# Performance work log

Measured on AMD Instinct MI355X. Metric: run time of the kernel, lower is better.

The kernel has to match this reference:

```python
import jax, jax.numpy as jnp
import numpy as np

N_EMBD = 1024
HEAD_SIZE = 64  # n_embd // n_head = 1024 // 16


def setup_inputs() -> dict:
    key = jax.random.key(0)
    ks = jax.random.split(key, 7)
    B, T, C, H = 4, 2048, N_EMBD, HEAD_SIZE
    s = 1.0 / np.sqrt(C)
    return {
        "x": jax.random.normal(ks[0], (B, T, C), dtype=jnp.float32),
        "Wq": jax.random.normal(ks[1], (C, H), dtype=jnp.float32) * s,
        "bq": jax.random.normal(ks[2], (H,), dtype=jnp.float32) * 0.01,
        "Wk": jax.random.normal(ks[3], (C, H), dtype=jnp.float32) * s,
        "bk": jax.random.normal(ks[4], (H,), dtype=jnp.float32) * 0.01,
        "Wv": jax.random.normal(ks[5], (C, H), dtype=jnp.float32) * s,
        "bv": jax.random.normal(ks[6], (H,), dtype=jnp.float32) * 0.01,
    }


def reference(x, Wq, bq, Wk, bk, Wv, bv):
    # x: [B, T, C]
    B, T, C = x.shape
    q = x @ Wq + bq  # [B, T, H]
    k = x @ Wk + bk  # [B, T, H]
    v = x @ Wv + bv  # [B, T, H]
    # NOTE: original module does NOT scale by 1/sqrt(head_size)
    wei = jnp.einsum("bth,bsh->bts", q, k)  # [B, T, T]
    causal = jnp.tril(jnp.ones((T, T), dtype=bool))
    wei = jnp.where(causal, wei, -jnp.inf)
    wei = jax.nn.softmax(wei, axis=-1)
    out = jnp.einsum("bts,bsh->bth", wei, v)  # [B, T, H]
    return out
```

## Files before the change

kernel.cpp:

```cpp
#include <hip/hip_runtime.h>

typedef float f32x4 __attribute__((ext_vector_type(4)));
typedef short s16x4 __attribute__((ext_vector_type(4)));
typedef short s16x8 __attribute__((ext_vector_type(8)));

#define LOG2E 1.4426950408889634f

__device__ __forceinline__ short f2bf(float f) {
  unsigned u = __float_as_uint(f);
  unsigned r = (u + 0x7fffu + ((u >> 16) & 1u)) >> 16;
  return (short)r;
}
__device__ __forceinline__ float bf2f(short s) {
  return __uint_as_float(((unsigned)(unsigned short)s) << 16);
}
__device__ __forceinline__ unsigned cvt_pk_bf16(float a, float b) {
  unsigned r;
  asm("v_cvt_pk_bf16_f32 %0, %1, %2" : "=v"(r) : "v"(a), "v"(b));
  return r;
}

__device__ __forceinline__ f32x4 mfma16(s16x4 a, s16x4 b, f32x4 c) {
  return __builtin_amdgcn_mfma_f32_16x16x16bf16_1k(a, b, c, 0, 0, 0);
}
__device__ __forceinline__ f32x4 mfma32(s16x8 a, s16x8 b, f32x4 c) {
  return __builtin_amdgcn_mfma_f32_16x16x32_bf16(a, b, c, 0, 0, 0);
}

__device__ __forceinline__ void gl_lds16(const void* gp, void* sp) {
  __builtin_amdgcn_global_load_lds(
      (__attribute__((address_space(1))) void*)const_cast<void*>(gp),
      (__attribute__((address_space(3))) void*)sp, 16, 0, 0);
}

__global__ __launch_bounds__(256) void prep_w(
    const float* __restrict__ Wq, const float* __restrict__ Wk, const float* __restrict__ Wv,
    short* __restrict__ wt_hi, short* __restrict__ wt_lo) {
  int idx = blockIdx.x * 256 + threadIdx.x;
  int n = idx >> 10;
  int c = idx & 1023;
  const float* W = (n < 64) ? Wq : ((n < 128) ? Wk : Wv);
  float v = W[c * 64 + (n & 63)];
  short hi = f2bf(v);
  short lo = f2bf(v - bf2f(hi));
  wt_hi[idx] = hi;
  wt_lo[idx] = lo;
}

__global__ __launch_bounds__(512, 2) void proj_qkv(
    const float* __restrict__ x,
    const short* __restrict__ wt_hi, const short* __restrict__ wt_lo,
    const float* __restrict__ bq, const float* __restrict__ bk, const float* __restrict__ bv,
    short* __restrict__ q_hi, short* __restrict__ q_lo,
    short* __restrict__ k_hi, short* __restrict__ k_lo,
    short* __restrict__ v_t) {
  const int tid = threadIdx.x;
  const int lane = tid & 63;
  const int wv = tid >> 6;
  const int col = lane & 15;
  const int g = lane >> 4;
  const int mg = wv >> 2;
  const int ng = wv & 3;
  const int tokbase = blockIdx.x * 32;

  __shared__ short lds[5][12288];

  const int wsl = ((lane & 3) ^ ((lane >> 3) & 3)) * 8;
  const short* s0 = wt_hi + (size_t)(16 * wv + (lane >> 2)) * 1024 + wsl;
  const int d0 = wv * 512;
  const int c1 = wv + 8;
  const short* s1 = (c1 < 12 ? wt_hi + (size_t)(16 * c1 + (lane >> 2)) * 1024
                             : wt_lo + (size_t)(16 * (c1 - 12) + (lane >> 2)) * 1024) + wsl;
  const int d1 = (c1 < 12) ? c1 * 512 : 6144 + (c1 - 12) * 512;
  const int c2 = wv + 16;
  const bool isx = (c2 >= 20);
  const short* s2 = isx
      ? (const short*)(x + (size_t)(tokbase + 8 * (c2 - 20) + (lane >> 3)) * 1024 +
                       ((lane & 7) ^ (lane >> 3)) * 4)
      : wt_lo + (size_t)(16 * (c2 - 12) + (lane >> 2)) * 1024 + wsl;
  const int d2 = isx ? 10240 + (c2 - 20) * 512 : 6144 + (c2 - 12) * 512;
  const int st2 = isx ? 64 : 32;

#define STAGE(BP, S) do { \
    gl_lds16(s0 + (S) * 32, (BP) + d0); \
    gl_lds16(s1 + (S) * 32, (BP) + d1); \
    gl_lds16(s2 + (S) * st2, (BP) + d2); \
  } while (0)

#define PIPE_WAIT(N) do { \
    asm volatile("s_waitcnt vmcnt(" #N ")" ::: "memory"); \
    __builtin_amdgcn_s_barrier(); \
    __builtin_amdgcn_sched_barrier(0); \
  } while (0)
#define PIPE_END do { \
    asm volatile("s_waitcnt lgkmcnt(0)" ::: "memory"); \
    __builtin_amdgcn_sched_barrier(0); \
    __builtin_amdgcn_s_barrier(); \
  } while (0)

  const int arow = mg * 16 + col;
  const int xq0 = ((2 * g) ^ (arow & 7)) << 2;
  const int xq1 = ((2 * g + 1) ^ (arow & 7)) << 2;
  const int rq = ng * 16 + col;
  const int ws = (g ^ ((rq >> 1) & 3)) << 3;

  f32x4 accQ = {0,0,0,0}, accK = {0,0,0,0}, accV = {0,0,0,0};

  typedef union { unsigned u[4]; s16x8 v8; } pk8;

#define COMPUTE(BP) do { \
    const short* bp_ = (BP); \
    const float* xb_ = (const float*)(bp_ + 10240); \
    f32x4 x0_ = *(const f32x4*)(xb_ + arow * 32 + xq0); \
    f32x4 x1_ = *(const f32x4*)(xb_ + arow * 32 + xq1); \
    pk8 xh_, xl_; \
    xh_.u[0] = cvt_pk_bf16(x0_[0], x0_[1]); \
    xh_.u[1] = cvt_pk_bf16(x0_[2], x0_[3]); \
    xh_.u[2] = cvt_pk_bf16(x1_[0], x1_[1]); \
    xh_.u[3] = cvt_pk_bf16(x1_[2], x1_[3]); \
    xl_.u[0] = cvt_pk_bf16(x0_[0] - __uint_as_float(xh_.u[0] << 16), \
                           x0_[1] - __uint_as_float(xh_.u[0] & 0xffff0000u)); \
    xl_.u[1] = cvt_pk_bf16(x0_[2] - __uint_as_float(xh_.u[1] << 16), \
                           x0_[3] - __uint_as_float(xh_.u[1] & 0xffff0000u)); \
    xl_.u[2] = cvt_pk_bf16(x1_[0] - __uint_as_float(xh_.u[2] << 16), \
                           x1_[1] - __uint_as_float(xh_.u[2] & 0xffff0000u)); \
    xl_.u[3] = cvt_pk_bf16(x1_[2] - __uint_as_float(xh_.u[3] << 16), \
                           x1_[3] - __uint_as_float(xh_.u[3] & 0xffff0000u)); \
    s16x8 qh_ = *(const s16x8*)(bp_ + rq * 32 + ws); \
    s16x8 kh_ = *(const s16x8*)(bp_ + (64 + rq) * 32 + ws); \
    s16x8 vh_ = *(const s16x8*)(bp_ + (128 + rq) * 32 + ws); \
    s16x8 ql_ = *(const s16x8*)(bp_ + 6144 + rq * 32 + ws); \
    s16x8 kl_ = *(const s16x8*)(bp_ + 6144 + (64 + rq) * 32 + ws); \
    accQ = mfma32(xh_.v8, qh_, accQ); \
    accK = mfma32(xh_.v8, kh_, accK); \
    accV = mfma32(xh_.v8, vh_, accV); \
    accQ = mfma32(xl_.v8, qh_, accQ); \
    accK = mfma32(xl_.v8, kh_, accK); \
    accQ = mfma32(xh_.v8, ql_, accQ); \
    accK = mfma32(xh_.v8, kl_, accK); \
  } while (0)

  short* cA = &lds[0][0];
  short* cB = &lds[1][0];
  short* cC = &lds[2][0];
  short* cD = &lds[3][0];
  short* cE = &lds[4][0];

  STAGE(cA, 0); STAGE(cB, 1); STAGE(cC, 2); STAGE(cD, 3);

#pragma unroll 1
  for (int b = 0; b < 28; ++b) {
    STAGE(cE, b + 4);
    PIPE_WAIT(12);
    COMPUTE(cA);
    PIPE_END;
    short* t = cA; cA = cB; cB = cC; cC = cD; cD = cE; cE = t;
  }
  PIPE_WAIT(9); COMPUTE(cA); PIPE_END;
  PIPE_WAIT(6); COMPUTE(cB); PIPE_END;
  PIPE_WAIT(3); COMPUTE(cC); PIPE_END;
  PIPE_WAIT(0); COMPUTE(cD);

  {
    const int hQ = ng * 16 + col;
    const float biasq = bq[hQ];
    const float biask = bk[hQ];
    const float biasv = bv[hQ];
#pragma unroll
    for (int r = 0; r < 4; ++r) {
      const int tok = tokbase + mg * 16 + 4 * g + r;
      float fq = accQ[r] + biasq;
      short qh = f2bf(fq);
      q_hi[(size_t)tok * 64 + hQ] = qh;
      q_lo[(size_t)tok * 64 + hQ] = f2bf(fq - bf2f(qh));
      float fk = accK[r] + biask;
      short kh = f2bf(fk);
      k_hi[(size_t)tok * 64 + hQ] = kh;
      k_lo[(size_t)tok * 64 + hQ] = f2bf(fk - bf2f(kh));
      const int bb = tok >> 11;
      const int tl = tok & 2047;
      v_t[((size_t)bb * 64 + hQ) * 2048 + tl] = f2bf(accV[r] + biasv);
    }
  }
#undef STAGE
#undef PIPE_WAIT
#undef PIPE_END
#undef COMPUTE
}

__global__ __launch_bounds__(256) void attn(
    const short* __restrict__ q_hi, const short* __restrict__ q_lo,
    const short* __restrict__ k_hi, const short* __restrict__ k_lo,
    const short* __restrict__ v_t,
    float* __restrict__ pm, float* __restrict__ pl, float* __restrict__ pO) {
  const int tid = threadIdx.x;
  const int lane = tid & 63;
  const int w = tid >> 6;
  const int col = lane & 15;
  const int g = lane >> 4;
  const int bid = blockIdx.x;
  const int p = bid & 31;
  const int b = (bid >> 5) & 3;
  const int s = bid >> 7;
  const int kb0 = 512 * s;
  if (kb0 > 64 * p + 63) return;
  const int S = (((64 * p + 63 - kb0) >> 5) + 1) < 16
                    ? (((64 * p + 63 - kb0) >> 5) + 1) : 16;

  __shared__ short lds[2][6144];

  const int qlo = 64 * p + 16 * w;

  const short* qbh = q_hi + (size_t)(b * 2048 + qlo + col) * 64 + g * 8;
  const short* qbl = q_lo + (size_t)(b * 2048 + qlo + col) * 64 + g * 8;
  s16x8 qh0 = *(const s16x8*)(qbh);
  s16x8 qh1 = *(const s16x8*)(qbh + 32);
  s16x8 ql0 = *(const s16x8*)(qbl);
  s16x8 ql1 = *(const s16x8*)(qbl + 32);
  asm volatile("" : "+v"(qh0), "+v"(qh1), "+v"(ql0), "+v"(ql1));

  f32x4 o0 = {0,0,0,0}, o1 = {0,0,0,0}, o2 = {0,0,0,0}, o3 = {0,0,0,0};
  float m = -3.0e38f, l = 0.0f;

  const int kr32 = 8 * w + (lane >> 3);
  const int ksl = ((lane & 7) ^ (lane >> 3)) * 8;
  const short* khs = k_hi + (size_t)(b * 2048 + kb0 + kr32) * 64 + ksl;
  const short* kls = k_lo + (size_t)(b * 2048 + kb0 + kr32) * 64 + ksl;
  const int vh_r = 16 * w + (lane >> 2);
  const int vsl = ((2 * (lane & 3)) ^ (vh_r & 6)) * 4;
  const short* vs = v_t + ((size_t)b * 64 + vh_r) * 2048 + kb0 + vsl;

#define STAGE(J) do { \
    short* bp_ = &lds[(J) & 1][0]; \
    gl_lds16(khs + (J) * 32 * 64, bp_ + w * 512); \
    gl_lds16(kls + (J) * 32 * 64, bp_ + 2048 + w * 512); \
    gl_lds16(vs + (J) * 32, bp_ + 4096 + w * 512); \
  } while (0)

  const int cx = col & 7;
  const int kslot0 = (g ^ cx) << 3;
  const int kslot1 = ((4 + g) ^ cx) << 3;
  const int vg0 = ((g) ^ (col & 6)) << 2;
  const int vg1 = ((4 + g) ^ (col & 6)) << 2;

#define SUBTILE(BP, KG0, VGOFF) do { \
    const short* kr_ = (BP) + ((KG0)&31) * 64 + col * 64; \
    s16x8 kh0_ = *(const s16x8*)(kr_ + kslot0); \
    s16x8 kh1_ = *(const s16x8*)(kr_ + kslot1); \
    s16x8 kl0_ = *(const s16x8*)(kr_ + 2048 + kslot0); \
    s16x8 kl1_ = *(const s16x8*)(kr_ + 2048 + kslot1); \
    f32x4 u1_ = {0,0,0,0}, u2_ = {0,0,0,0}; \
    u1_ = mfma32(kh0_, qh0, u1_); u1_ = mfma32(kh1_, qh1, u1_); \
    u2_ = mfma32(kh0_, ql0, u2_); u2_ = mfma32(kh1_, ql1, u2_); \
    u2_ = mfma32(kl0_, qh0, u2_); u2_ = mfma32(kl1_, qh1, u2_); \
    f32x4 s_ = u1_ + u2_; \
    if ((KG0) == qlo) { \
      _Pragma("unroll") for (int i = 0; i < 4; ++i) \
        if (4 * g + i > col) s_[i] = -3.0e38f; \
    } \
    float mx_ = fmaxf(fmaxf(s_[0], s_[1]), fmaxf(s_[2], s_[3])); \
    mx_ = fmaxf(mx_, __shfl_xor(mx_, 16)); \
    mx_ = fmaxf(mx_, __shfl_xor(mx_, 32)); \
    const float mn_ = fmaxf(m, mx_); \
    const float rs_ = __builtin_amdgcn_exp2f((m - mn_) * LOG2E); \
    const float p0_ = __builtin_amdgcn_exp2f((s_[0] - mn_) * LOG2E); \
    const float p1_ = __builtin_amdgcn_exp2f((s_[1] - mn_) * LOG2E); \
    const float p2_ = __builtin_amdgcn_exp2f((s_[2] - mn_) * LOG2E); \
    const float p3_ = __builtin_amdgcn_exp2f((s_[3] - mn_) * LOG2E); \
    l = l * rs_ + (p0_ + p1_ + p2_ + p3_); \
    o0 *= rs_; o1 *= rs_; o2 *= rs_; o3 *= rs_; \
    m = mn_; \
    s16x4 pb_; \
    pb_[0] = f2bf(p0_); pb_[1] = f2bf(p1_); pb_[2] = f2bf(p2_); pb_[3] = f2bf(p3_); \
    const short* vb_ = (BP) + 4096 + col * 32 + (VGOFF); \
    o0 = mfma16(*(const s16x4*)(vb_),        pb_, o0); \
    o1 = mfma16(*(const s16x4*)(vb_ + 512),  pb_, o1); \
    o2 = mfma16(*(const s16x4*)(vb_ + 1024), pb_, o2); \
    o3 = mfma16(*(const s16x4*)(vb_ + 1536), pb_, o3); \
  } while (0)

#define COMPUTE(J) do { \
    const int kb_ = kb0 + 32 * (J); \
    if (kb_ <= qlo + 15) { \
      const short* bp_ = &lds[(J) & 1][0]; \
      SUBTILE(bp_, kb_, vg0); \
      if (kb_ + 16 <= qlo + 15) SUBTILE(bp_, kb_ + 16, vg1); \
    } \
  } while (0)

  STAGE(0);
  __syncthreads();
#pragma unroll 1
  for (int j = 0; j < S; ++j) {
    if (j + 1 < S) STAGE(j + 1);
    COMPUTE(j);
    __syncthreads();
  }

  l += __shfl_xor(l, 16);
  l += __shfl_xor(l, 32);
  const int row = b * 2048 + qlo + col;
  if (g == 0) {
    pm[s * 8192 + row] = m;
    pl[s * 8192 + row] = l;
  }
  {
    float* d = pO + ((size_t)s * 8192 + row) * 64 + 4 * g;
    *(f32x4*)(d)      = o0;
    *(f32x4*)(d + 16) = o1;
    *(f32x4*)(d + 32) = o2;
    *(f32x4*)(d + 48) = o3;
  }
#undef STAGE
#undef SUBTILE
#undef COMPUTE
}

__global__ __launch_bounds__(256) void reduce_p(
    const float* __restrict__ pm, const float* __restrict__ pl,
    const float* __restrict__ pO, float* __restrict__ out) {
  const int idx = blockIdx.x * 256 + threadIdx.x;
  const int row = idx >> 4;
  const int hq = (idx & 15) * 4;
  const int smax = (row & 2047) >> 9;
  float M = -3.0e38f;
  for (int s = 0; s <= smax; ++s) M = fmaxf(M, pm[s * 8192 + row]);
  float L = 0.f;
  f32x4 acc = {0, 0, 0, 0};
  for (int s = 0; s <= smax; ++s) {
    const float ws = __builtin_amdgcn_exp2f((pm[s * 8192 + row] - M) * LOG2E);
    L += ws * pl[s * 8192 + row];
    f32x4 ov = *(const f32x4*)(pO + ((size_t)s * 8192 + row) * 64 + hq);
    acc += ov * ws;
  }
  const float invL = 1.0f / L;
  *(f32x4*)(out + (size_t)row * 64 + hq) = acc * invL;
}

extern "C" void kernel_launch(void* const* d_in, const int* in_sizes, int n_in,
                              void* d_out, int out_size, void* d_ws, size_t ws_size,
                              hipStream_t stream) {
  const float* x  = (const float*)d_in[0];
  const float* Wq = (const float*)d_in[1];
  const float* bq = (const float*)d_in[2];
  const float* Wk = (const float*)d_in[3];
  const float* bk = (const float*)d_in[4];
  const float* Wv = (const float*)d_in[5];
  const float* bv = (const float*)d_in[6];
  float* out = (float*)d_out;

  char* ws = (char*)d_ws;
  short* wt_hi = (short*)(ws);
  short* wt_lo = (short*)(ws + 393216);
  short* q_hi  = (short*)(ws + 786432);
  short* q_lo  = (short*)(ws + 786432 + 1048576);
  short* k_hi  = (short*)(ws + 786432 + 2 * 1048576);
  short* k_lo  = (short*)(ws + 786432 + 3 * 1048576);
  short* v_t   = (short*)(ws + 786432 + 4 * 1048576);
  float* pm    = (float*)(ws + 6029312);
  float* pl    = (float*)(ws + 6160384);
  float* pO    = (float*)(ws + 6291456);

  hipLaunchKernelGGL(prep_w, dim3(768), dim3(256), 0, stream, Wq, Wk, Wv, wt_hi, wt_lo);
  hipLaunchKernelGGL(proj_qkv, dim3(256), dim3(512), 0, stream,
                     x, wt_hi, wt_lo, bq, bk, bv, q_hi, q_lo, k_hi, k_lo, v_t);
  hipLaunchKernelGGL(attn, dim3(512), dim3(256), 0, stream,
                     q_hi, q_lo, k_hi, k_lo, v_t, pm, pl, pO);
  hipLaunchKernelGGL(reduce_p, dim3(512), dim3(256), 0, stream, pm, pl, pO, out);
}
```

Measured before the change: 57.57 us.

## Split attention into two-pass softmax kernel writing P and separate PV kernel

Replaces the flash-style online-softmax attention plus split-K reduction with two kernels. The first computes QK scores twice, once to find the per-warp row max and again to write bf16 exponentials to a materialized P buffer in global memory along with per-warp max and sum. The second multiplies P by V and merges the 8 warp partials through LDS. This removes the rescaling of O on every tile and the separate reduce kernel, but it doubles the QK MFMA work, drops LDS staging of K/V, and adds a large P write and read through global memory.

Measured after the change: 86.99 us. 51.1% more time.

```diff
diff --git a/kernel.cpp b/kernel.cpp
--- a/kernel.cpp
+++ b/kernel.cpp
@@ -188,153 +188,202 @@
 #undef COMPUTE
 }
 
-__global__ __launch_bounds__(256) void attn(
+__global__ __launch_bounds__(512) void qk_p(
     const short* __restrict__ q_hi, const short* __restrict__ q_lo,
     const short* __restrict__ k_hi, const short* __restrict__ k_lo,
-    const short* __restrict__ v_t,
-    float* __restrict__ pm, float* __restrict__ pl, float* __restrict__ pO) {
+    short* __restrict__ P, float* __restrict__ pm, float* __restrict__ pl) {
   const int tid = threadIdx.x;
   const int lane = tid & 63;
   const int w = tid >> 6;
   const int col = lane & 15;
   const int g = lane >> 4;
-  const int bid = blockIdx.x;
-  const int p = bid & 31;
-  const int b = (bid >> 5) & 3;
-  const int s = bid >> 7;
-  const int kb0 = 512 * s;
-  if (kb0 > 64 * p + 63) return;
-  const int S = (((64 * p + 63 - kb0) >> 5) + 1) < 16
-                    ? (((64 * p + 63 - kb0) >> 5) + 1) : 16;
-
-  __shared__ short lds[2][6144];
-
-  const int qlo = 64 * p + 16 * w;
-
-  const short* qbh = q_hi + (size_t)(b * 2048 + qlo + col) * 64 + g * 8;
-  const short* qbl = q_lo + (size_t)(b * 2048 + qlo + col) * 64 + g * 8;
-  s16x8 qh0 = *(const s16x8*)(qbh);
-  s16x8 qh1 = *(const s16x8*)(qbh + 32);
-  s16x8 ql0 = *(const s16x8*)(qbl);
-  s16x8 ql1 = *(const s16x8*)(qbl + 32);
-  asm volatile("" : "+v"(qh0), "+v"(qh1), "+v"(ql0), "+v"(ql1));
-
-  f32x4 o0 = {0,0,0,0}, o1 = {0,0,0,0}, o2 = {0,0,0,0}, o3 = {0,0,0,0};
-  float m = -3.0e38f, l = 0.0f;
-
-  const int kr32 = 8 * w + (lane >> 3);
-  const int ksl = ((lane & 7) ^ (lane >> 3)) * 8;
-  const short* khs = k_hi + (size_t)(b * 2048 + kb0 + kr32) * 64 + ksl;
-  const short* kls = k_lo + (size_t)(b * 2048 + kb0 + kr32) * 64 + ksl;
-  const int vh_r = 16 * w + (lane >> 2);
-  const int vsl = ((2 * (lane & 3)) ^ (vh_r & 6)) * 4;
-  const short* vs = v_t + ((size_t)b * 64 + vh_r) * 2048 + kb0 + vsl;
-
-#define STAGE(J) do { \
-    short* bp_ = &lds[(J) & 1][0]; \
-    gl_lds16(khs + (J) * 32 * 64, bp_ + w * 512); \
-    gl_lds16(kls + (J) * 32 * 64, bp_ + 2048 + w * 512); \
-    gl_lds16(vs + (J) * 32, bp_ + 4096 + w * 512); \
-  } while (0)
-
-  const int cx = col & 7;
-  const int kslot0 = (g ^ cx) << 3;
-  const int kslot1 = ((4 + g) ^ cx) << 3;
-  const int vg0 = ((g) ^ (col & 6)) << 2;
-  const int vg1 = ((4 + g) ^ (col & 6)) << 2;
-
-#define SUBTILE(BP, KG0, VGOFF) do { \
-    const short* kr_ = (BP) + ((KG0)&31) * 64 + col * 64; \
-    s16x8 kh0_ = *(const s16x8*)(kr_ + kslot0); \
-    s16x8 kh1_ = *(const s16x8*)(kr_ + kslot1); \
-    s16x8 kl0_ = *(const s16x8*)(kr_ + 2048 + kslot0); \
-    s16x8 kl1_ = *(const s16x8*)(kr_ + 2048 + kslot1); \
+  const int T = 63 - (blockIdx.x >> 2);
+  const int b = blockIdx.x & 3;
+  const int t0 = 2 * T, t1 = 2 * T + 1;
+
+  const short* q0h = q_hi + (size_t)(b * 2048 + t0 * 16 + col) * 64 + g * 8;
+  const short* q0l = q_lo + (size_t)(b * 2048 + t0 * 16 + col) * 64 + g * 8;
+  s16x8 qh00 = *(const s16x8*)(q0h);
+  s16x8 qh01 = *(const s16x8*)(q0h + 32);
+  s16x8 ql00 = *(const s16x8*)(q0l);
+  s16x8 ql01 = *(const s16x8*)(q0l + 32);
+  s16x8 qh10 = *(const s16x8*)(q0h + 16 * 64);
+  s16x8 qh11 = *(const s16x8*)(q0h + 16 * 64 + 32);
+  s16x8 ql10 = *(const s16x8*)(q0l + 16 * 64);
+  s16x8 ql11 = *(const s16x8*)(q0l + 16 * 64 + 32);
+  asm volatile("" : "+v"(qh00), "+v"(qh01), "+v"(ql00), "+v"(ql01));
+  asm volatile("" : "+v"(qh10), "+v"(qh11), "+v"(ql10), "+v"(ql11));
+
+#define SCORES(OUT, QH0, QH1, QL0, QL1, TT, KT) do { \
     f32x4 u1_ = {0,0,0,0}, u2_ = {0,0,0,0}; \
-    u1_ = mfma32(kh0_, qh0, u1_); u1_ = mfma32(kh1_, qh1, u1_); \
-    u2_ = mfma32(kh0_, ql0, u2_); u2_ = mfma32(kh1_, ql1, u2_); \
-    u2_ = mfma32(kl0_, qh0, u2_); u2_ = mfma32(kl1_, qh1, u2_); \
-    f32x4 s_ = u1_ + u2_; \
-    if ((KG0) == qlo) { \
+    u1_ = mfma32(kh0_, QH0, u1_); u1_ = mfma32(kh1_, QH1, u1_); \
+    u2_ = mfma32(kh0_, QL0, u2_); u2_ = mfma32(kh1_, QL1, u2_); \
+    u2_ = mfma32(kl0_, QH0, u2_); u2_ = mfma32(kl1_, QH1, u2_); \
+    OUT = u1_ + u2_; \
+    if ((KT) == (TT)) { \
       _Pragma("unroll") for (int i = 0; i < 4; ++i) \
-        if (4 * g + i > col) s_[i] = -3.0e38f; \
+        if (4 * g + i > col) OUT[i] = -3.0e38f; \
     } \
-    float mx_ = fmaxf(fmaxf(s_[0], s_[1]), fmaxf(s_[2], s_[3])); \
-    mx_ = fmaxf(mx_, __shfl_xor(mx_, 16)); \
-    mx_ = fmaxf(mx_, __shfl_xor(mx_, 32)); \
-    const float mn_ = fmaxf(m, mx_); \
-    const float rs_ = __builtin_amdgcn_exp2f((m - mn_) * LOG2E); \
-    const float p0_ = __builtin_amdgcn_exp2f((s_[0] - mn_) * LOG2E); \
-    const float p1_ = __builtin_amdgcn_exp2f((s_[1] - mn_) * LOG2E); \
-    const float p2_ = __builtin_amdgcn_exp2f((s_[2] - mn_) * LOG2E); \
-    const float p3_ = __builtin_amdgcn_exp2f((s_[3] - mn_) * LOG2E); \
-    l = l * rs_ + (p0_ + p1_ + p2_ + p3_); \
-    o0 *= rs_; o1 *= rs_; o2 *= rs_; o3 *= rs_; \
-    m = mn_; \
-    s16x4 pb_; \
-    pb_[0] = f2bf(p0_); pb_[1] = f2bf(p1_); pb_[2] = f2bf(p2_); pb_[3] = f2bf(p3_); \
-    const short* vb_ = (BP) + 4096 + col * 32 + (VGOFF); \
-    o0 = mfma16(*(const s16x4*)(vb_),        pb_, o0); \
-    o1 = mfma16(*(const s16x4*)(vb_ + 512),  pb_, o1); \
-    o2 = mfma16(*(const s16x4*)(vb_ + 1024), pb_, o2); \
-    o3 = mfma16(*(const s16x4*)(vb_ + 1536), pb_, o3); \
-  } while (0)
-
-#define COMPUTE(J) do { \
-    const int kb_ = kb0 + 32 * (J); \
-    if (kb_ <= qlo + 15) { \
-      const short* bp_ = &lds[(J) & 1][0]; \
-      SUBTILE(bp_, kb_, vg0); \
-      if (kb_ + 16 <= qlo + 15) SUBTILE(bp_, kb_ + 16, vg1); \
+  } while (0)
+
+  float m0 = -3.0e38f, m1 = -3.0e38f;
+
+#pragma unroll 1
+  for (int kt = w; kt <= t1; kt += 8) {
+    const short* krh = k_hi + (size_t)(b * 2048 + kt * 16 + col) * 64 + g * 8;
+    const short* krl = k_lo + (size_t)(b * 2048 + kt * 16 + col) * 64 + g * 8;
+    s16x8 kh0_ = *(const s16x8*)(krh);
+    s16x8 kh1_ = *(const s16x8*)(krh + 32);
+    s16x8 kl0_ = *(const s16x8*)(krl);
+    s16x8 kl1_ = *(const s16x8*)(krl + 32);
+    f32x4 s_;
+    SCORES(s_, qh10, qh11, ql10, ql11, t1, kt);
+    m1 = fmaxf(m1, fmaxf(fmaxf(s_[0], s_[1]), fmaxf(s_[2], s_[3])));
+    if (kt <= t0) {
+      SCORES(s_, qh00, qh01, ql00, ql01, t0, kt);
+      m0 = fmaxf(m0, fmaxf(fmaxf(s_[0], s_[1]), fmaxf(s_[2], s_[3])));
+    }
+  }
+  m0 = fmaxf(m0, __shfl_xor(m0, 16));
+  m0 = fmaxf(m0, __shfl_xor(m0, 32));
+  m1 = fmaxf(m1, __shfl_xor(m1, 16));
+  m1 = fmaxf(m1, __shfl_xor(m1, 32));
+
+  float lw0 = 0.0f, lw1 = 0.0f;
+
+#pragma unroll 1
+  for (int kt = w; kt <= t1; kt += 8) {
+    const short* krh = k_hi + (size_t)(b * 2048 + kt * 16 + col) * 64 + g * 8;
+    const short* krl = k_lo + (size_t)(b * 2048 + kt * 16 + col) * 64 + g * 8;
+    s16x8 kh0_ = *(const s16x8*)(krh);
+    s16x8 kh1_ = *(const s16x8*)(krh + 32);
+    s16x8 kl0_ = *(const s16x8*)(krl);
+    s16x8 kl1_ = *(const s16x8*)(krl + 32);
+    f32x4 s_;
+    __builtin_amdgcn_s_setprio(1);
+    SCORES(s_, qh10, qh11, ql10, ql11, t1, kt);
+    __builtin_amdgcn_s_setprio(0);
+    {
+      const float p0 = __builtin_amdgcn_exp2f((s_[0] - m1) * LOG2E);
+      const float p1 = __builtin_amdgcn_exp2f((s_[1] - m1) * LOG2E);
+      const float p2 = __builtin_amdgcn_exp2f((s_[2] - m1) * LOG2E);
+      const float p3 = __builtin_amdgcn_exp2f((s_[3] - m1) * LOG2E);
+      lw1 += p0 + p1 + p2 + p3;
+      s16x4 pb;
+      pb[0] = f2bf(p0); pb[1] = f2bf(p1); pb[2] = f2bf(p2); pb[3] = f2bf(p3);
+      *(s16x4*)(P + ((size_t)((b * 128 + t1) * 128 + kt)) * 256 + col * 16 + 4 * g) = pb;
+    }
+    if (kt <= t0) {
+      __builtin_amdgcn_s_setprio(1);
+      SCORES(s_, qh00, qh01, ql00, ql01, t0, kt);
+      __builtin_amdgcn_s_setprio(0);
+      const float p0 = __builtin_amdgcn_exp2f((s_[0] - m0) * LOG2E);
+      const float p1 = __builtin_amdgcn_exp2f((s_[1] - m0) * LOG2E);
+      const float p2 = __builtin_amdgcn_exp2f((s_[2] - m0) * LOG2E);
+      const float p3 = __builtin_amdgcn_exp2f((s_[3] - m0) * LOG2E);
+      lw0 += p0 + p1 + p2 + p3;
+      s16x4 pb;
+      pb[0] = f2bf(p0); pb[1] = f2bf(p1); pb[2] = f2bf(p2); pb[3] = f2bf(p3);
+      *(s16x4*)(P + ((size_t)((b * 128 + t0) * 128 + kt)) * 256 + col * 16 + 4 * g) = pb;
+    }
+  }
+  lw0 += __shfl_xor(lw0, 16); lw0 += __shfl_xor(lw0, 32);
+  lw1 += __shfl_xor(lw1, 16); lw1 += __shfl_xor(lw1, 32);
+
+  if (g == 0) {
+    pm[w * 8192 + b * 2048 + t0 * 16 + col] = m0;
+    pl[w * 8192 + b * 2048 + t0 * 16 + col] = lw0;
+    pm[w * 8192 + b * 2048 + t1 * 16 + col] = m1;
+    pl[w * 8192 + b * 2048 + t1 * 16 + col] = lw1;
+  }
+#undef SCORES
+}
+
+__global__ __launch_bounds__(512) void pv(
+    const short* __restrict__ P, const short* __restrict__ v_t,
+    const float* __restrict__ pm, const float* __restrict__ pl,
+    float* __restrict__ out) {
+  const int tid = threadIdx.x;
+  const int lane = tid & 63;
+  const int w = tid >> 6;
+  const int col = lane & 15;
+  const int g = lane >> 4;
+  const int T = 63 - (blockIdx.x >> 2);
+  const int b = blockIdx.x & 3;
+  const int t0 = 2 * T, t1 = 2 * T + 1;
+
+  __shared__ float ldsO[8 * 64 * 17];
+
+  f32x4 o00 = {0,0,0,0}, o01 = {0,0,0,0}, o02 = {0,0,0,0}, o03 = {0,0,0,0};
+  f32x4 o10 = {0,0,0,0}, o11 = {0,0,0,0}, o12 = {0,0,0,0}, o13 = {0,0,0,0};
+
+  const short* vbase = v_t + ((size_t)b * 64 + col) * 2048 + 4 * g;
+
+#pragma unroll 1
+  for (int kt = w; kt <= t1; kt += 8) {
+    const short* vr = vbase + 16 * kt;
+    s16x4 v0 = *(const s16x4*)(vr);
+    s16x4 v1 = *(const s16x4*)(vr + 16 * 2048);
+    s16x4 v2 = *(const s16x4*)(vr + 32 * 2048);
+    s16x4 v3 = *(const s16x4*)(vr + 48 * 2048);
+    s16x4 pb1 = *(const s16x4*)(P + ((size_t)((b * 128 + t1) * 128 + kt)) * 256 + col * 16 + 4 * g);
+    __builtin_amdgcn_s_setprio(1);
+    o10 = mfma16(v0, pb1, o10);
+    o11 = mfma16(v1, pb1, o11);
+    o12 = mfma16(v2, pb1, o12);
+    o13 = mfma16(v3, pb1, o13);
+    __builtin_amdgcn_s_setprio(0);
+    if (kt <= t0) {
+      s16x4 pb0 = *(const s16x4*)(P + ((size_t)((b * 128 + t0) * 128 + kt)) * 256 + col * 16 + 4 * g);
+      __builtin_amdgcn_s_setprio(1);
+      o00 = mfma16(v0, pb0, o00);
+      o01 = mfma16(v1, pb0, o01);
+      o02 = mfma16(v2, pb0, o02);
+      o03 = mfma16(v3, pb0, o03);
+      __builtin_amdgcn_s_setprio(0);
+    }
+  }
+
+#define MERGE(TT, O0, O1, O2, O3) do { \
+    _Pragma("unroll") \
+    for (int r = 0; r < 4; ++r) { \
+      ldsO[(w * 64 +  0 + 4 * g + r) * 17 + col] = O0[r]; \
+      ldsO[(w * 64 + 16 + 4 * g + r) * 17 + col] = O1[r]; \
+      ldsO[(w * 64 + 32 + 4 * g + r) * 17 + col] = O2[r]; \
+      ldsO[(w * 64 + 48 + 4 * g + r) * 17 + col] = O3[r]; \
     } \
-  } while (0)
-
-  STAGE(0);
-  __syncthreads();
-#pragma unroll 1
-  for (int j = 0; j < S; ++j) {
-    if (j + 1 < S) STAGE(j + 1);
-    COMPUTE(j);
-    __syncthreads();
-  }
-
-  l += __shfl_xor(l, 16);
-  l += __shfl_xor(l, 32);
-  const int row = b * 2048 + qlo + col;
-  if (g == 0) {
-    pm[s * 8192 + row] = m;
-    pl[s * 8192 + row] = l;
-  }
-  {
-    float* d = pO + ((size_t)s * 8192 + row) * 64 + 4 * g;
-    *(f32x4*)(d)      = o0;
-    *(f32x4*)(d + 16) = o1;
-    *(f32x4*)(d + 32) = o2;
-    *(f32x4*)(d + 48) = o3;
-  }
-#undef STAGE
-#undef SUBTILE
-#undef COMPUTE
-}
-
-__global__ __launch_bounds__(256) void reduce_p(
-    const float* __restrict__ pm, const float* __restrict__ pl,
-    const float* __restrict__ pO, float* __restrict__ out) {
-  const int idx = blockIdx.x * 256 + threadIdx.x;
-  const int row = idx >> 4;
-  const int hq = (idx & 15) * 4;
-  const int smax = (row & 2047) >> 9;
-  float M = -3.0e38f;
-  for (int s = 0; s <= smax; ++s) M = fmaxf(M, pm[s * 8192 + row]);
-  float L = 0.f;
-  f32x4 acc = {0, 0, 0, 0};
-  for (int s = 0; s <= smax; ++s) {
-    const float ws = __builtin_amdgcn_exp2f((pm[s * 8192 + row] - M) * LOG2E);
-    L += ws * pl[s * 8192 + row];
-    f32x4 ov = *(const f32x4*)(pO + ((size_t)s * 8192 + row) * 64 + hq);
-    acc += ov * ws;
-  }
-  const float invL = 1.0f / L;
-  *(f32x4*)(out + (size_t)row * 64 + hq) = acc * invL;
+    __syncthreads(); \
+    { \
+      const int q = tid >> 5;           \
+      const int h0 = tid & 31;          \
+      const int row = b * 2048 + (TT) * 16 + q; \
+      float mw[8], lw[8]; \
+      _Pragma("unroll") \
+      for (int u = 0; u < 8; ++u) { mw[u] = pm[u * 8192 + row]; lw[u] = pl[u * 8192 + row]; } \
+      float M = mw[0]; \
+      _Pragma("unroll") for (int u = 1; u < 8; ++u) M = fmaxf(M, mw[u]); \
+      float ew[8]; float L = 0.0f; \
+      _Pragma("unroll") \
+      for (int u = 0; u < 8; ++u) { \
+        ew[u] = __builtin_amdgcn_exp2f((mw[u] - M) * LOG2E); \
+        L += ew[u] * lw[u]; \
+      } \
+      const float invL = 1.0f / L; \
+      _Pragma("unroll") \
+      for (int e = 0; e < 2; ++e) { \
+        const int h = h0 + 32 * e; \
+        float acc = 0.0f; \
+        _Pragma("unroll") \
+        for (int u = 0; u < 8; ++u) acc += ew[u] * ldsO[(u * 64 + h) * 17 + q]; \
+        out[(size_t)row * 64 + h] = acc * invL; \
+      } \
+    } \
+    __syncthreads(); \
+  } while (0)
+
+  MERGE(t0, o00, o01, o02, o03);
+  MERGE(t1, o10, o11, o12, o13);
+#undef MERGE
 }
 
 extern "C" void kernel_launch(void* const* d_in, const int* in_sizes, int n_in,
@@ -357,14 +406,15 @@
   short* k_hi  = (short*)(ws + 786432 + 2 * 1048576);
   short* k_lo  = (short*)(ws + 786432 + 3 * 1048576);
   short* v_t   = (short*)(ws + 786432 + 4 * 1048576);
-  float* pm    = (float*)(ws + 6029312);
-  float* pl    = (float*)(ws + 6160384);
-  float* pO    = (float*)(ws + 6291456);
+  short* Pbuf  = (short*)(ws + 6029312);
+  float* pm    = (float*)(ws + 39583744);
+  float* pl    = (float*)(ws + 39845888);
 
   hipLaunchKernelGGL(prep_w, dim3(768), dim3(256), 0, stream, Wq, Wk, Wv, wt_hi, wt_lo);
   hipLaunchKernelGGL(proj_qkv, dim3(256), dim3(512), 0, stream,
                      x, wt_hi, wt_lo, bq, bk, bv, q_hi, q_lo, k_hi, k_lo, v_t);
-  hipLaunchKernelGGL(attn, dim3(512), dim3(256), 0, stream,
-                     q_hi, q_lo, k_hi, k_lo, v_t, pm, pl, pO);
-  hipLaunchKernelGGL(reduce_p, dim3(512), dim3(256), 0, stream, pm, pl, pO, out);
-}
+  hipLaunchKernelGGL(qk_p, dim3(256), dim3(512), 0, stream,
+                     q_hi, q_lo, k_hi, k_lo, Pbuf, pm, pl);
+  hipLaunchKernelGGL(pv, dim3(256), dim3(512), 0, stream,
+                     Pbuf, v_t, pm, pl, out);
+}
```

## Split attention into per-wave 128-key chunks reading K/V directly from global memory

Applied to the files above, without the earlier changes.

Rewrites the attention kernel so each wave independently handles one 16-row query tile against one 128-key chunk (8 subtiles), with 16 chunks per row instead of 4. The LDS double-buffered staging and block barriers are removed, and K and V are loaded straight from global memory, relying on cache reuse across waves. Fully masked chunks write neutral partials, and the reduction and workspace offsets are resized for 16 splits. This exposes much more parallelism and removes sync, at the cost of more partial-output traffic in the reduce step and uncoalesced, uncached-in-LDS global loads.

Result: slower. 106.6 us (+85.2%).

```diff
diff --git a/kernel.cpp b/kernel.cpp
--- a/kernel.cpp
+++ b/kernel.cpp
@@ -193,26 +193,35 @@
     const short* __restrict__ k_hi, const short* __restrict__ k_lo,
     const short* __restrict__ v_t,
     float* __restrict__ pm, float* __restrict__ pl, float* __restrict__ pO) {
-  const int tid = threadIdx.x;
-  const int lane = tid & 63;
-  const int w = tid >> 6;
+  const int lane = threadIdx.x & 63;
+  const int w = threadIdx.x >> 6;
   const int col = lane & 15;
   const int g = lane >> 4;
-  const int bid = blockIdx.x;
-  const int p = bid & 31;
-  const int b = (bid >> 5) & 3;
-  const int s = bid >> 7;
-  const int kb0 = 512 * s;
-  if (kb0 > 64 * p + 63) return;
-  const int S = (((64 * p + 63 - kb0) >> 5) + 1) < 16
-                    ? (((64 * p + 63 - kb0) >> 5) + 1) : 16;
-
-  __shared__ short lds[2][6144];
-
-  const int qlo = 64 * p + 16 * w;
-
-  const short* qbh = q_hi + (size_t)(b * 2048 + qlo + col) * 64 + g * 8;
-  const short* qbl = q_lo + (size_t)(b * 2048 + qlo + col) * 64 + g * 8;
+  const int W = blockIdx.x * 4 + w;
+  const int c = W & 15;
+  const int t = (W >> 4) & 127;
+  const int b = W >> 11;
+  const int kbase = b * 2048;
+  const int row = kbase + t * 16 + col;
+  float* dO = pO + ((size_t)c * 8192 + row) * 64 + 4 * g;
+
+  if (8 * c > t) {
+    if (g == 0) {
+      pm[c * 8192 + row] = -3.0e38f;
+      pl[c * 8192 + row] = 0.0f;
+    }
+    const f32x4 z = {0.f, 0.f, 0.f, 0.f};
+    *(f32x4*)(dO)      = z;
+    *(f32x4*)(dO + 16) = z;
+    *(f32x4*)(dO + 32) = z;
+    *(f32x4*)(dO + 48) = z;
+    return;
+  }
+  const int ks0 = 8 * c;
+  const int ks1 = (8 * c + 7 < t) ? 8 * c + 7 : t;
+
+  const short* qbh = q_hi + (size_t)(row) * 64 + g * 8;
+  const short* qbl = q_lo + (size_t)(row) * 64 + g * 8;
   s16x8 qh0 = *(const s16x8*)(qbh);
   s16x8 qh1 = *(const s16x8*)(qbh + 32);
   s16x8 ql0 = *(const s16x8*)(qbl);
@@ -222,98 +231,65 @@
   f32x4 o0 = {0,0,0,0}, o1 = {0,0,0,0}, o2 = {0,0,0,0}, o3 = {0,0,0,0};
   float m = -3.0e38f, l = 0.0f;
 
-  const int kr32 = 8 * w + (lane >> 3);
-  const int ksl = ((lane & 7) ^ (lane >> 3)) * 8;
-  const short* khs = k_hi + (size_t)(b * 2048 + kb0 + kr32) * 64 + ksl;
-  const short* kls = k_lo + (size_t)(b * 2048 + kb0 + kr32) * 64 + ksl;
-  const int vh_r = 16 * w + (lane >> 2);
-  const int vsl = ((2 * (lane & 3)) ^ (vh_r & 6)) * 4;
-  const short* vs = v_t + ((size_t)b * 64 + vh_r) * 2048 + kb0 + vsl;
-
-#define STAGE(J) do { \
-    short* bp_ = &lds[(J) & 1][0]; \
-    gl_lds16(khs + (J) * 32 * 64, bp_ + w * 512); \
-    gl_lds16(kls + (J) * 32 * 64, bp_ + 2048 + w * 512); \
-    gl_lds16(vs + (J) * 32, bp_ + 4096 + w * 512); \
-  } while (0)
-
-  const int cx = col & 7;
-  const int kslot0 = (g ^ cx) << 3;
-  const int kslot1 = ((4 + g) ^ cx) << 3;
-  const int vg0 = ((g) ^ (col & 6)) << 2;
-  const int vg1 = ((4 + g) ^ (col & 6)) << 2;
-
-#define SUBTILE(BP, KG0, VGOFF) do { \
-    const short* kr_ = (BP) + ((KG0)&31) * 64 + col * 64; \
-    s16x8 kh0_ = *(const s16x8*)(kr_ + kslot0); \
-    s16x8 kh1_ = *(const s16x8*)(kr_ + kslot1); \
-    s16x8 kl0_ = *(const s16x8*)(kr_ + 2048 + kslot0); \
-    s16x8 kl1_ = *(const s16x8*)(kr_ + 2048 + kslot1); \
-    f32x4 u1_ = {0,0,0,0}, u2_ = {0,0,0,0}; \
-    u1_ = mfma32(kh0_, qh0, u1_); u1_ = mfma32(kh1_, qh1, u1_); \
-    u2_ = mfma32(kh0_, ql0, u2_); u2_ = mfma32(kh1_, ql1, u2_); \
-    u2_ = mfma32(kl0_, qh0, u2_); u2_ = mfma32(kl1_, qh1, u2_); \
-    f32x4 s_ = u1_ + u2_; \
-    if ((KG0) == qlo) { \
-      _Pragma("unroll") for (int i = 0; i < 4; ++i) \
-        if (4 * g + i > col) s_[i] = -3.0e38f; \
+#define SUBTILE(KT) do { \
+    if ((KT) <= ks1) { \
+      const short* krh_ = k_hi + (size_t)(kbase + (KT) * 16 + col) * 64 + g * 8; \
+      const short* krl_ = k_lo + (size_t)(kbase + (KT) * 16 + col) * 64 + g * 8; \
+      s16x8 kh0_ = *(const s16x8*)(krh_); \
+      s16x8 kh1_ = *(const s16x8*)(krh_ + 32); \
+      s16x8 kl0_ = *(const s16x8*)(krl_); \
+      s16x8 kl1_ = *(const s16x8*)(krl_ + 32); \
+      f32x4 u1_ = {0,0,0,0}, u2_ = {0,0,0,0}; \
+      u1_ = mfma32(kh0_, qh0, u1_); u1_ = mfma32(kh1_, qh1, u1_); \
+      u2_ = mfma32(kh0_, ql0, u2_); u2_ = mfma32(kh1_, ql1, u2_); \
+      u2_ = mfma32(kl0_, qh0, u2_); u2_ = mfma32(kl1_, qh1, u2_); \
+      f32x4 s_ = u1_ + u2_; \
+      if ((KT) == t) { \
+        _Pragma("unroll") for (int ii = 0; ii < 4; ++ii) \
+          if (4 * g + ii > col) s_[ii] = -3.0e38f; \
+      } \
+      float mx_ = fmaxf(fmaxf(s_[0], s_[1]), fmaxf(s_[2], s_[3])); \
+      mx_ = fmaxf(mx_, __shfl_xor(mx_, 16)); \
+      mx_ = fmaxf(mx_, __shfl_xor(mx_, 32)); \
+      const float mn_ = fmaxf(m, mx_); \
+      const float rs_ = __builtin_amdgcn_exp2f((m - mn_) * LOG2E); \
+      const float p0_ = __builtin_amdgcn_exp2f((s_[0] - mn_) * LOG2E); \
+      const float p1_ = __builtin_amdgcn_exp2f((s_[1] - mn_) * LOG2E); \
+      const float p2_ = __builtin_amdgcn_exp2f((s_[2] - mn_) * LOG2E); \
+      const float p3_ = __builtin_amdgcn_exp2f((s_[3] - mn_) * LOG2E); \
+      l = l * rs_ + (p0_ + p1_ + p2_ + p3_); \
+      o0 *= rs_; o1 *= rs_; o2 *= rs_; o3 *= rs_; \
+      m = mn_; \
+      s16x4 pb_; \
+      pb_[0] = f2bf(p0_); pb_[1] = f2bf(p1_); pb_[2] = f2bf(p2_); pb_[3] = f2bf(p3_); \
+      const short* vr_ = v_t + ((size_t)b * 64 + col) * 2048 + (KT) * 16 + 4 * g; \
+      o0 = mfma16(*(const s16x4*)(vr_),             pb_, o0); \
+      o1 = mfma16(*(const s16x4*)(vr_ + 16 * 2048), pb_, o1); \
+      o2 = mfma16(*(const s16x4*)(vr_ + 32 * 2048), pb_, o2); \
+      o3 = mfma16(*(const s16x4*)(vr_ + 48 * 2048), pb_, o3); \
     } \
-    float mx_ = fmaxf(fmaxf(s_[0], s_[1]), fmaxf(s_[2], s_[3])); \
-    mx_ = fmaxf(mx_, __shfl_xor(mx_, 16)); \
-    mx_ = fmaxf(mx_, __shfl_xor(mx_, 32)); \
-    const float mn_ = fmaxf(m, mx_); \
-    const float rs_ = __builtin_amdgcn_exp2f((m - mn_) * LOG2E); \
-    const float p0_ = __builtin_amdgcn_exp2f((s_[0] - mn_) * LOG2E); \
-    const float p1_ = __builtin_amdgcn_exp2f((s_[1] - mn_) * LOG2E); \
-    const float p2_ = __builtin_amdgcn_exp2f((s_[2] - mn_) * LOG2E); \
-    const float p3_ = __builtin_amdgcn_exp2f((s_[3] - mn_) * LOG2E); \
-    l = l * rs_ + (p0_ + p1_ + p2_ + p3_); \
-    o0 *= rs_; o1 *= rs_; o2 *= rs_; o3 *= rs_; \
-    m = mn_; \
-    s16x4 pb_; \
-    pb_[0] = f2bf(p0_); pb_[1] = f2bf(p1_); pb_[2] = f2bf(p2_); pb_[3] = f2bf(p3_); \
-    const short* vb_ = (BP) + 4096 + col * 32 + (VGOFF); \
-    o0 = mfma16(*(const s16x4*)(vb_),        pb_, o0); \
-    o1 = mfma16(*(const s16x4*)(vb_ + 512),  pb_, o1); \
-    o2 = mfma16(*(const s16x4*)(vb_ + 1024), pb_, o2); \
-    o3 = mfma16(*(const s16x4*)(vb_ + 1536), pb_, o3); \
-  } while (0)
-
-#define COMPUTE(J) do { \
-    const int kb_ = kb0 + 32 * (J); \
-    if (kb_ <= qlo + 15) { \
-      const short* bp_ = &lds[(J) & 1][0]; \
-      SUBTILE(bp_, kb_, vg0); \
-      if (kb_ + 16 <= qlo + 15) SUBTILE(bp_, kb_ + 16, vg1); \
-    } \
-  } while (0)
-
-  STAGE(0);
-  __syncthreads();
-#pragma unroll 1
-  for (int j = 0; j < S; ++j) {
-    if (j + 1 < S) STAGE(j + 1);
-    COMPUTE(j);
-    __syncthreads();
-  }
+  } while (0)
+
+  SUBTILE(ks0);
+  SUBTILE(ks0 + 1);
+  SUBTILE(ks0 + 2);
+  SUBTILE(ks0 + 3);
+  SUBTILE(ks0 + 4);
+  SUBTILE(ks0 + 5);
+  SUBTILE(ks0 + 6);
+  SUBTILE(ks0 + 7);
 
   l += __shfl_xor(l, 16);
   l += __shfl_xor(l, 32);
-  const int row = b * 2048 + qlo + col;
   if (g == 0) {
-    pm[s * 8192 + row] = m;
-    pl[s * 8192 + row] = l;
-  }
-  {
-    float* d = pO + ((size_t)s * 8192 + row) * 64 + 4 * g;
-    *(f32x4*)(d)      = o0;
-    *(f32x4*)(d + 16) = o1;
-    *(f32x4*)(d + 32) = o2;
-    *(f32x4*)(d + 48) = o3;
-  }
-#undef STAGE
+    pm[c * 8192 + row] = m;
+    pl[c * 8192 + row] = l;
+  }
+  *(f32x4*)(dO)      = o0;
+  *(f32x4*)(dO + 16) = o1;
+  *(f32x4*)(dO + 32) = o2;
+  *(f32x4*)(dO + 48) = o3;
 #undef SUBTILE
-#undef COMPUTE
 }
 
 __global__ __launch_bounds__(256) void reduce_p(
@@ -322,12 +298,12 @@
   const int idx = blockIdx.x * 256 + threadIdx.x;
   const int row = idx >> 4;
   const int hq = (idx & 15) * 4;
-  const int smax = (row & 2047) >> 9;
+  const int ns = (((row & 2047) >> 4) >> 3) + 1;
   float M = -3.0e38f;
-  for (int s = 0; s <= smax; ++s) M = fmaxf(M, pm[s * 8192 + row]);
+  for (int s = 0; s < ns; ++s) M = fmaxf(M, pm[s * 8192 + row]);
   float L = 0.f;
   f32x4 acc = {0, 0, 0, 0};
-  for (int s = 0; s <= smax; ++s) {
+  for (int s = 0; s < ns; ++s) {
     const float ws = __builtin_amdgcn_exp2f((pm[s * 8192 + row] - M) * LOG2E);
     L += ws * pl[s * 8192 + row];
     f32x4 ov = *(const f32x4*)(pO + ((size_t)s * 8192 + row) * 64 + hq);
@@ -358,13 +334,13 @@
   short* k_lo  = (short*)(ws + 786432 + 3 * 1048576);
   short* v_t   = (short*)(ws + 786432 + 4 * 1048576);
   float* pm    = (float*)(ws + 6029312);
-  float* pl    = (float*)(ws + 6160384);
-  float* pO    = (float*)(ws + 6291456);
+  float* pl    = (float*)(ws + 6553600);
+  float* pO    = (float*)(ws + 7077888);
 
   hipLaunchKernelGGL(prep_w, dim3(768), dim3(256), 0, stream, Wq, Wk, Wv, wt_hi, wt_lo);
   hipLaunchKernelGGL(proj_qkv, dim3(256), dim3(512), 0, stream,
                      x, wt_hi, wt_lo, bq, bk, bv, q_hi, q_lo, k_hi, k_lo, v_t);
-  hipLaunchKernelGGL(attn, dim3(512), dim3(256), 0, stream,
+  hipLaunchKernelGGL(attn, dim3(2048), dim3(256), 0, stream,
                      q_hi, q_lo, k_hi, k_lo, v_t, pm, pl, pO);
   hipLaunchKernelGGL(reduce_p, dim3(512), dim3(256), 0, stream, pm, pl, pO, out);
 }
```
